# Kernel tuning notes

Hardware: AMD Instinct MI355X
Metric: run time of the kernel (lower is better)

The kernel has to match this reference:

```python
import jax, jax.numpy as jnp
import numpy as np

NUM_CLASSES = 21
TOP_K = 200
VAR0, VAR1 = 0.1, 0.2
CONF_THRESH = 0.01
NMS_THRESH = 0.45
NUM_PRIORS = 3000
BATCH = 256


def _decode(loc, priors):
    # loc, priors: [P, 4] (cx, cy, w, h) -> corner boxes [P, 4]
    cxcy = priors[:, :2] + loc[:, :2] * VAR0 * priors[:, 2:]
    wh = priors[:, 2:] * jnp.exp(loc[:, 2:] * VAR1)
    return jnp.concatenate([cxcy - wh * 0.5, cxcy + wh * 0.5], axis=1)


def _iou_one_vs_all(box, boxes):
    # box [4], boxes [P,4] corner form
    lt = jnp.maximum(box[:2], boxes[:, :2])
    rb = jnp.minimum(box[2:], boxes[:, 2:])
    wh = jnp.clip(rb - lt, 0.0)
    inter = wh[:, 0] * wh[:, 1]
    area1 = (box[2] - box[0]) * (box[3] - box[1])
    area2 = (boxes[:, 2] - boxes[:, 0]) * (boxes[:, 3] - boxes[:, 1])
    return inter / (area1 + area2 - inter)


def _nms_one_class(boxes, scores):
    # boxes [P,4], scores [P] -> [TOP_K, 5] rows of (score, x1, y1, x2, y2)
    neg_inf = jnp.array(-jnp.inf, boxes.dtype)
    sc0 = jnp.where(scores > CONF_THRESH, scores, neg_inf)

    def step(sc, _):
        i = jnp.argmax(sc)
        s = sc[i]
        b = boxes[i]
        valid = s > CONF_THRESH
        iou = _iou_one_vs_all(b, boxes)
        sc = jnp.where(iou > NMS_THRESH, neg_inf, sc).at[i].set(neg_inf)
        row = jnp.where(valid, jnp.concatenate([s[None], b]), jnp.zeros(5, boxes.dtype))
        return sc, row

    _, rows = jax.lax.scan(step, sc0, None, length=TOP_K)
    return rows


def setup_inputs() -> dict:
    key = jax.random.key(0)
    k1, k2, k3 = jax.random.split(key, 3)
    loc_data = jax.random.normal(k1, (BATCH, NUM_PRIORS, 4), dtype=jnp.float32)
    conf_data = jax.random.uniform(k2, (BATCH, NUM_PRIORS, NUM_CLASSES), dtype=jnp.float32)
    pr = jax.random.uniform(k3, (NUM_PRIORS, 4), dtype=jnp.float32)
    # centers in [0,1], widths/heights in [0.05, 0.5]
    priors = jnp.concatenate([pr[:, :2], 0.05 + 0.45 * pr[:, 2:]], axis=1)
    return {"loc_data": loc_data, "conf_data": conf_data, "priors": priors}


def reference(loc_data, conf_data, priors):
    # decode per image: [B, P, 4]
    decoded = jax.vmap(lambda l: _decode(l, priors))(loc_data)
    # class-major scores, skipping background class 0: [B, C-1, P]
    cls_scores = jnp.transpose(conf_data, (0, 2, 1))[:, 1:, :]
    per_bc = jax.vmap(jax.vmap(_nms_one_class, in_axes=(None, 0)),
                      in_axes=(0, 0))(decoded, cls_scores)  # [B, C-1, TOP_K, 5]
    bg = jnp.zeros((loc_data.shape[0], 1, TOP_K, 5), loc_data.dtype)
    return jnp.concatenate([bg, per_bc], axis=1)  # [B, C, TOP_K, 5]
```

## Files before the change

### kernel.cpp

```cpp
#include <hip/hip_runtime.h>
#include <math.h>


#define NCLS 21
#define TOPK 200
#define NPRI 3000
#define ELTS 47
#define CONF_T 0.01f
#define MHI 0.45f
#define MLO 1.490116119384765625e-08f
#define CAP 256
#define NBUCK 256
#define NUSED 224
#define BITS_BASE 0x3C000000u
#define BSHIFT 18

__device__ __forceinline__ float rdlf(float v, int l) {
  return __int_as_float(__builtin_amdgcn_readlane(__float_as_int(v), l));
}

__device__ __forceinline__ float iou_val(const float4 k, const float a,
                                         const float4 b, const float carea) {
  float ltx = fmaxf(k.x, b.x), lty = fmaxf(k.y, b.y);
  float rbx = fminf(k.z, b.z), rby = fminf(k.w, b.w);
  float iw = fmaxf(rbx - ltx, 0.0f), ih = fmaxf(rby - lty, 0.0f);
  float inter = iw * ih;
  float uni = (a + carea) - inter;
  return fmaf(-MLO, uni, fmaf(-MHI, uni, inter));
}

__device__ __forceinline__ bool iou_sup(const float4 k, const float a,
                                        const float4 b, const float carea) {
  return iou_val(k, a, b, carea) > 0.0f;
}

__device__ __forceinline__ int resolve_tile(
    unsigned long long smask, const float4 bx, const float carea,
    const unsigned int bits, const int lane, int nk,
    float4* kbox, float* karr, float* kscore) {
  unsigned long long M = ~smask;
  while (M && nk < TOPK) {
    const int ls = (int)__builtin_ctzll(M);
    const float sx1 = rdlf(bx.x, ls), sy1 = rdlf(bx.y, ls);
    const float sx2 = rdlf(bx.z, ls), sy2 = rdlf(bx.w, ls);
    const float sar = rdlf(carea, ls);
    const unsigned int sbits =
        (unsigned int)__builtin_amdgcn_readlane((int)bits, ls);
    const float4 nb = make_float4(sx1, sy1, sx2, sy2);
    if (lane == 0) {
      kbox[nk]   = nb;
      karr[nk]   = sar;
      kscore[nk] = __uint_as_float(sbits);
    }
    ++nk;
    M &= ~__ballot(iou_val(nb, sar, bx, carea) > 0.0f);
    M &= ~(1ull << ls);
  }
  return nk;
}

__global__ void decode_kernel(const float* __restrict__ loc,
                              const float* __restrict__ priors,
                              float4* __restrict__ wsbox,
                              float* __restrict__ out) {
  const int b = blockIdx.x;
  float* o0 = out + (size_t)b * NCLS * TOPK * 5;
  for (int i = threadIdx.x; i < TOPK * 5; i += 256) o0[i] = 0.0f;
  for (int j = threadIdx.x; j < NPRI; j += 256) {
    const float4 l4 = *(const float4*)(loc + ((size_t)b * NPRI + j) * 4);
    const float4 p  = *(const float4*)(priors + (size_t)j * 4);
    float cx = p.x + (l4.x * 0.1f) * p.z;
    float cy = p.y + (l4.y * 0.1f) * p.w;
    float bw = p.z * expf(l4.z * 0.2f);
    float bh = p.w * expf(l4.w * 0.2f);
    wsbox[(size_t)b * NPRI + j] = make_float4(cx - bw * 0.5f, cy - bh * 0.5f,
                                              cx + bw * 0.5f, cy + bh * 0.5f);
  }
}

__global__ __launch_bounds__(128, 8) void ssd_nms_kernel(
    const float* __restrict__ conf, const float4* __restrict__ wsbox,
    float* __restrict__ out, int nbatch) {
  const int blk = blockIdx.x;
  int b, c1;
  if ((nbatch & 7) == 0) {
    const int xcd  = blk & 7;
    const int rest = blk >> 3;
    b  = (rest / 20) * 8 + xcd;
    c1 = rest % 20;
  } else {
    b  = blk / 20;
    c1 = blk % 20;
  }
  const int c    = 1 + c1;
  const int tid  = threadIdx.x;
  const int lane = tid & 63;
  const int w    = tid >> 6;

  __shared__ unsigned long long skey[CAP];
  __shared__ unsigned int hist[NBUCK / 2];
  __shared__ float4 kbox[TOPK];
  __shared__ alignas(16) float karr[TOPK];
  __shared__ float  kscore[TOPK];
  __shared__ int sh_nk;
  __shared__ int sh_ctr;

  for (int i = tid; i < NBUCK / 2; i += 128) hist[i] = 0u;
  if (tid == 0) sh_nk = 0;
  __syncthreads();

  const float* myF = conf + (size_t)b * NPRI * NCLS + c;

  for (int k = w; k < ELTS; k += 2) {
    const int j = k * 64 + lane;
    unsigned int bits = 0u;
    if (j < NPRI) {
      float s = myF[(size_t)j * NCLS];
      bits = (s > CONF_T) ? __float_as_uint(s) : 0u;
    }
    if (bits) {
      unsigned int bu = (bits - BITS_BASE) >> BSHIFT;
      atomicAdd(&hist[bu >> 1], 1u << ((bu & 1) * 16));
    }
  }
  __syncthreads();

  float* obase = out + ((size_t)b * NCLS + c) * (TOPK * 5);
  const float4* mybox = wsbox + (size_t)b * NPRI;
  int cutHiB = NUSED;

  for (;;) {
    if (sh_nk >= TOPK || cutHiB <= 0) break;

    int sl = 0;
#pragma unroll
    for (int t = 0; t < 4; ++t) {
      int bu = lane * 4 + t;
      if (bu < cutHiB) sl += (int)((hist[bu >> 1] >> ((bu & 1) * 16)) & 0xFFFFu);
    }
    int suf = sl;
#pragma unroll
    for (int d = 1; d < 64; d <<= 1) {
      int v = __shfl_down(suf, d, 64);
      if (lane + d < 64) suf += v;
    }
    unsigned long long m = __ballot(suf <= CAP);
    int Ls = (m != 0ull) ? __builtin_ctzll(m) : 63;
    int cutLoB = Ls * 4;
    if (cutLoB >= cutHiB) cutLoB = (cutHiB - 1) & ~3;
    const unsigned int loBits = BITS_BASE + ((unsigned)cutLoB << BSHIFT);
    const unsigned int hiBits = BITS_BASE + ((unsigned)cutHiB << BSHIFT);

    if (tid == 0) sh_ctr = 0;
    for (int t = tid; t < CAP; t += 128) skey[t] = 0ull;
    __syncthreads();

    for (int k = w; k < ELTS; k += 2) {
      const int j = k * 64 + lane;
      unsigned int bits = 0u;
      if (j < NPRI) {
        float s = myF[(size_t)j * NCLS];
        bits = (s > CONF_T) ? __float_as_uint(s) : 0u;
      }
      bool sel = (bits >= loBits) && (bits < hiBits);
      unsigned long long bm = __ballot(sel);
      int cnt = (int)__popcll(bm);
      int wb = 0;
      if (lane == 0 && cnt) wb = atomicAdd(&sh_ctr, cnt);
      wb = __builtin_amdgcn_readfirstlane(wb);
      if (sel) {
        int pos = wb + (int)__popcll(bm & ((1ull << lane) - 1ull));
        if (pos < CAP)
          skey[pos] = ((unsigned long long)bits << 12) | (unsigned)(4095 - j);
      }
    }
    __syncthreads();
    int Nc = sh_ctr;
    if (Nc > CAP) Nc = CAP;

    if (Nc > 0) {
      for (int kk = 2; kk <= CAP; kk <<= 1) {
        for (int jj = kk >> 1; jj > 0; jj >>= 1) {
          if (jj == 128) __syncthreads();
          int i = ((tid & ~(jj - 1)) << 1) | (tid & (jj - 1));
          int ixj = i | jj;
          unsigned long long a = skey[i], d = skey[ixj];
          bool up = (i & kk) == 0;
          if (up ? (a < d) : (a > d)) { skey[i] = d; skey[ixj] = a; }
          if (jj == 128) __syncthreads();
          else __threadfence_block();
        }
      }
      __syncthreads();

      for (int p0 = 0;; p0 += 128) {
        if (p0 >= Nc) break;
        const int nk0 = sh_nk;
        if (nk0 >= TOPK) break;

        const int p = p0 + w * 64 + lane;
        const bool valid = p < Nc;
        unsigned long long key = valid ? skey[p] : 0ull;
        unsigned int bits = (unsigned int)(key >> 12);
        int j = 4095 - (int)(key & 4095ull);
        float4 bx = mybox[valid ? j : 0];
        float carea = (bx.z - bx.x) * (bx.w - bx.y);

        float fm = valid ? -1.0f : 1.0f;
        int s = 0;
        for (; s + 3 < nk0; s += 4) {
          float4 k0 = kbox[s];     float4 k1 = kbox[s + 1];
          float4 k2 = kbox[s + 2]; float4 k3 = kbox[s + 3];
          float4 ar = *(const float4*)&karr[s];
          float v01 = fmaxf(iou_val(k0, ar.x, bx, carea),
                            iou_val(k1, ar.y, bx, carea));
          float v23 = fmaxf(iou_val(k2, ar.z, bx, carea),
                            iou_val(k3, ar.w, bx, carea));
          fm = fmaxf(fm, fmaxf(v01, v23));
          if (__ballot(fm > 0.0f) == ~0ull) { s = nk0; break; }
        }
        for (; s < nk0; ++s)
          fm = fmaxf(fm, iou_val(kbox[s], karr[s], bx, carea));
        unsigned long long smask = __ballot(fm > 0.0f);

        if (w == 0) {
          int nk = resolve_tile(smask, bx, carea, bits, lane, nk0,
                                kbox, karr, kscore);
          if (lane == 0) sh_nk = nk;
        }
        __syncthreads();
        if (w == 1) {
          const int nk1 = sh_nk;
          for (int s2 = nk0; s2 < nk1; ++s2) {
            smask |= __ballot(iou_sup(kbox[s2], karr[s2], bx, carea));
            if (smask == ~0ull) break;
          }
          int nk = resolve_tile(smask, bx, carea, bits, lane, nk1,
                                kbox, karr, kscore);
          if (lane == 0) sh_nk = nk;
        }
        __syncthreads();
      }
    }
    cutHiB = cutLoB;
  }

  __syncthreads();
  const int nkf = sh_nk;
  const float* kbf = (const float*)&kbox[0];
  for (int i = tid; i < TOPK * 5; i += 128) {
    int r = i / 5;
    int col = i - r * 5;
    float v = 0.0f;
    if (r < nkf) v = (col == 0) ? kscore[r] : kbf[r * 4 + (col - 1)];
    obase[i] = v;
  }
}

extern "C" void kernel_launch(void* const* d_in, const int* in_sizes, int n_in,
                              void* d_out, int out_size, void* d_ws, size_t ws_size,
                              hipStream_t stream) {
  const float* loc    = (const float*)d_in[0];
  const float* conf   = (const float*)d_in[1];
  const float* priors = (const float*)d_in[2];
  float* out = (float*)d_out;
  float4* wsbox = (float4*)d_ws;

  const int batch = in_sizes[0] / (NPRI * 4);
  hipLaunchKernelGGL(decode_kernel, dim3(batch), dim3(256), 0, stream,
                     loc, priors, wsbox, out);
  hipLaunchKernelGGL(ssd_nms_kernel, dim3(batch * 20), dim3(128), 0, stream,
                     conf, wsbox, out, batch);
}
```

Before: 430.9 us.

## Process all 256 sorted candidates in one pass with two per lane

The candidate loop over 128-wide tiles becomes a single pass. Each of the two waves now holds two 64-candidate halves (A and B) per lane and checks both against the already-kept boxes in one sweep. A combined resolve routine takes kept boxes from A before B, in score order. This removes the extra tile iteration with its barriers and repeated kept-list scans, at the cost of more registers and always scanning the second half even when the first half would already reach TOPK.

```diff
diff --git a/kernel.cpp b/kernel.cpp
--- a/kernel.cpp
+++ b/kernel.cpp
@@ -29,32 +29,38 @@
   return fmaf(-MLO, uni, fmaf(-MHI, uni, inter));
 }
 
-__device__ __forceinline__ bool iou_sup(const float4 k, const float a,
-                                        const float4 b, const float carea) {
-  return iou_val(k, a, b, carea) > 0.0f;
-}
-
-__device__ __forceinline__ int resolve_tile(
-    unsigned long long smask, const float4 bx, const float carea,
-    const unsigned int bits, const int lane, int nk,
+__device__ __forceinline__ int resolve_tile2(
+    unsigned long long MA, unsigned long long MB,
+    const float4 bxA, const float caA, const unsigned int bitsA,
+    const float4 bxB, const float caB, const unsigned int bitsB,
+    const int lane, int nk,
     float4* kbox, float* karr, float* kscore) {
-  unsigned long long M = ~smask;
-  while (M && nk < TOPK) {
-    const int ls = (int)__builtin_ctzll(M);
-    const float sx1 = rdlf(bx.x, ls), sy1 = rdlf(bx.y, ls);
-    const float sx2 = rdlf(bx.z, ls), sy2 = rdlf(bx.w, ls);
-    const float sar = rdlf(carea, ls);
-    const unsigned int sbits =
-        (unsigned int)__builtin_amdgcn_readlane((int)bits, ls);
-    const float4 nb = make_float4(sx1, sy1, sx2, sy2);
+  while ((MA | MB) && nk < TOPK) {
+    const bool fromA = (MA != 0ull);
+    float4 nb; float nar; unsigned int nbits;
+    if (fromA) {
+      const int ls = (int)__builtin_ctzll(MA);
+      nb = make_float4(rdlf(bxA.x, ls), rdlf(bxA.y, ls),
+                       rdlf(bxA.z, ls), rdlf(bxA.w, ls));
+      nar = rdlf(caA, ls);
+      nbits = (unsigned int)__builtin_amdgcn_readlane((int)bitsA, ls);
+      MA &= ~(1ull << ls);
+    } else {
+      const int ls = (int)__builtin_ctzll(MB);
+      nb = make_float4(rdlf(bxB.x, ls), rdlf(bxB.y, ls),
+                       rdlf(bxB.z, ls), rdlf(bxB.w, ls));
+      nar = rdlf(caB, ls);
+      nbits = (unsigned int)__builtin_amdgcn_readlane((int)bitsB, ls);
+      MB &= ~(1ull << ls);
+    }
     if (lane == 0) {
       kbox[nk]   = nb;
-      karr[nk]   = sar;
-      kscore[nk] = __uint_as_float(sbits);
+      karr[nk]   = nar;
+      kscore[nk] = __uint_as_float(nbits);
     }
     ++nk;
-    M &= ~__ballot(iou_val(nb, sar, bx, carea) > 0.0f);
-    M &= ~(1ull << ls);
+    MA &= ~__ballot(iou_val(nb, nar, bxA, caA) > 0.0f);
+    MB &= ~__ballot(iou_val(nb, nar, bxB, caB) > 0.0f);
   }
   return nk;
 }
@@ -193,54 +199,68 @@
       }
       __syncthreads();
 
-      for (int p0 = 0;; p0 += 128) {
-        if (p0 >= Nc) break;
-        const int nk0 = sh_nk;
-        if (nk0 >= TOPK) break;
-
-        const int p = p0 + w * 64 + lane;
-        const bool valid = p < Nc;
-        unsigned long long key = valid ? skey[p] : 0ull;
-        unsigned int bits = (unsigned int)(key >> 12);
-        int j = 4095 - (int)(key & 4095ull);
-        float4 bx = mybox[valid ? j : 0];
-        float carea = (bx.z - bx.x) * (bx.w - bx.y);
-
-        float fm = valid ? -1.0f : 1.0f;
-        int s = 0;
-        for (; s + 3 < nk0; s += 4) {
-          float4 k0 = kbox[s];     float4 k1 = kbox[s + 1];
-          float4 k2 = kbox[s + 2]; float4 k3 = kbox[s + 3];
-          float4 ar = *(const float4*)&karr[s];
-          float v01 = fmaxf(iou_val(k0, ar.x, bx, carea),
-                            iou_val(k1, ar.y, bx, carea));
-          float v23 = fmaxf(iou_val(k2, ar.z, bx, carea),
-                            iou_val(k3, ar.w, bx, carea));
-          fm = fmaxf(fm, fmaxf(v01, v23));
-          if (__ballot(fm > 0.0f) == ~0ull) { s = nk0; break; }
+      const int nk0 = sh_nk;
+
+      const int pA = w * 128 + lane;
+      const int pB = pA + 64;
+      const bool vA = pA < Nc, vB = pB < Nc;
+      unsigned long long keyA = vA ? skey[pA] : 0ull;
+      unsigned long long keyB = vB ? skey[pB] : 0ull;
+      unsigned int bitsA = (unsigned int)(keyA >> 12);
+      unsigned int bitsB = (unsigned int)(keyB >> 12);
+      int jA = 4095 - (int)(keyA & 4095ull);
+      int jB = 4095 - (int)(keyB & 4095ull);
+      float4 bxA = mybox[vA ? jA : 0];
+      float4 bxB = mybox[vB ? jB : 0];
+      float caA = (bxA.z - bxA.x) * (bxA.w - bxA.y);
+      float caB = (bxB.z - bxB.x) * (bxB.w - bxB.y);
+
+      float fmA = vA ? -1.0f : 1.0f;
+      float fmB = vB ? -1.0f : 1.0f;
+      int s = 0;
+      for (; s + 3 < nk0; s += 4) {
+        float4 k0 = kbox[s];     float4 k1 = kbox[s + 1];
+        float4 k2 = kbox[s + 2]; float4 k3 = kbox[s + 3];
+        float4 ar = *(const float4*)&karr[s];
+        float a01 = fmaxf(iou_val(k0, ar.x, bxA, caA),
+                          iou_val(k1, ar.y, bxA, caA));
+        float a23 = fmaxf(iou_val(k2, ar.z, bxA, caA),
+                          iou_val(k3, ar.w, bxA, caA));
+        fmA = fmaxf(fmA, fmaxf(a01, a23));
+        float b01 = fmaxf(iou_val(k0, ar.x, bxB, caB),
+                          iou_val(k1, ar.y, bxB, caB));
+        float b23 = fmaxf(iou_val(k2, ar.z, bxB, caB),
+                          iou_val(k3, ar.w, bxB, caB));
+        fmB = fmaxf(fmB, fmaxf(b01, b23));
+        if (__ballot(fmA > 0.0f && fmB > 0.0f) == ~0ull) { s = nk0; break; }
+      }
+      for (; s < nk0; ++s) {
+        float4 kk = kbox[s]; float ka = karr[s];
+        fmA = fmaxf(fmA, iou_val(kk, ka, bxA, caA));
+        fmB = fmaxf(fmB, iou_val(kk, ka, bxB, caB));
+      }
+      unsigned long long sA = __ballot(fmA > 0.0f);
+      unsigned long long sB = __ballot(fmB > 0.0f);
+
+      if (w == 0) {
+        int nk = resolve_tile2(~sA, ~sB, bxA, caA, bitsA, bxB, caB, bitsB,
+                               lane, nk0, kbox, karr, kscore);
+        if (lane == 0) sh_nk = nk;
+      }
+      __syncthreads();
+      if (w == 1) {
+        const int nk1 = sh_nk;
+        for (int s2 = nk0; s2 < nk1; ++s2) {
+          float4 kk = kbox[s2]; float ka = karr[s2];
+          sA |= __ballot(iou_val(kk, ka, bxA, caA) > 0.0f);
+          sB |= __ballot(iou_val(kk, ka, bxB, caB) > 0.0f);
+          if ((sA & sB) == ~0ull) break;
         }
-        for (; s < nk0; ++s)
-          fm = fmaxf(fm, iou_val(kbox[s], karr[s], bx, carea));
-        unsigned long long smask = __ballot(fm > 0.0f);
-
-        if (w == 0) {
-          int nk = resolve_tile(smask, bx, carea, bits, lane, nk0,
-                                kbox, karr, kscore);
-          if (lane == 0) sh_nk = nk;
-        }
-        __syncthreads();
-        if (w == 1) {
-          const int nk1 = sh_nk;
-          for (int s2 = nk0; s2 < nk1; ++s2) {
-            smask |= __ballot(iou_sup(kbox[s2], karr[s2], bx, carea));
-            if (smask == ~0ull) break;
-          }
-          int nk = resolve_tile(smask, bx, carea, bits, lane, nk1,
-                                kbox, karr, kscore);
-          if (lane == 0) sh_nk = nk;
-        }
-        __syncthreads();
-      }
+        int nk = resolve_tile2(~sA, ~sB, bxA, caA, bitsA, bxB, caB, bitsB,
+                               lane, nk1, kbox, karr, kscore);
+        if (lane == 0) sh_nk = nk;
+      }
+      __syncthreads();
     }
     cutHiB = cutLoB;
   }
```

Measured after the change: 500.4 us. 16.1% more time.
